# Optimization experiments

Hardware: AMD Instinct MI355X
Metric: run time of the kernel (lower is better)

The kernel has to match this reference:

```python
import jax, jax.numpy as jnp
import numpy as np

VOCAB = 4096   # vocab_size; must equal dim for weight + A@B to typecheck (as in source)
DIM = 4096
RANK = 256     # lora_rank
BATCH, SEQ = 4, 2048


def setup_inputs() -> dict:
    key = jax.random.key(0)
    k1, k2, k3, k4, k5 = jax.random.split(key, 5)
    x = jax.random.randint(k1, (BATCH, SEQ), 0, VOCAB)
    padding_mask = jax.random.randint(k2, (BATCH, SEQ), 0, 2).astype(bool)
    weight = jax.random.normal(k3, (VOCAB, DIM), dtype=jnp.float32) * 0.02
    A = jax.random.normal(k4, (VOCAB, RANK), dtype=jnp.float32) * 0.01
    B = jax.random.normal(k5, (RANK, VOCAB), dtype=jnp.float32) * 0.01
    return {"x": x, "padding_mask": padding_mask, "weight": weight, "A": A, "B": B}


def reference(x, padding_mask, weight, A, B):
    # world_size == 1, rank == 0 in the source module, so the distributed
    # index-shift / mask / all_reduce branches are no-ops.
    # lora_rank > 0 branch: embedding against the LoRA-corrected weight.
    # NOTE: faithful to source, A@B is [V, V] and requires DIM == VOCAB.
    corrected = weight + A @ B            # [V, DIM]
    y = corrected[x]                      # gather rows -> [B, S, DIM]
    # y[padding_mask] = 0
    y = jnp.where(padding_mask[..., None], jnp.zeros((), dtype=y.dtype), y)
    return y
```

## Files before the change

kernel.cpp:

```cpp
#include <hip/hip_runtime.h>
#include <stdint.h>

#define NTOK 8192
#define NCOL 4096
#define RANK 256
#define TPB  128
#define CPB  256

typedef __attribute__((ext_vector_type(8))) short bf16x8;
typedef __attribute__((ext_vector_type(4))) float f32x4;

__device__ __forceinline__ unsigned short f2bf(float f) {
    unsigned int u = __float_as_uint(f);
    u += 0x7fffu + ((u >> 16) & 1u);
    return (unsigned short)(u >> 16);
}

__global__ __launch_bounds__(256) void prep_kernel(
    const float* __restrict__ A, const float* __restrict__ B,
    unsigned short* __restrict__ Abf, unsigned short* __restrict__ Bfrag)
{
    if (blockIdx.x < 1024) {
        int i = blockIdx.x * 256 + threadIdx.x;
        float4 v = reinterpret_cast<const float4*>(A)[i];
        ushort4 o;
        o.x = f2bf(v.x); o.y = f2bf(v.y); o.z = f2bf(v.z); o.w = f2bf(v.w);
        reinterpret_cast<ushort4*>(Abf)[i] = o;
    } else {
        int gt = (blockIdx.x - 1024) * 256 + threadIdx.x;
        int ct = gt >> 9;
        int rem = gt & 511;
        int ks = rem >> 6;
        int ln = rem & 63;
        int col = ct * 16 + (ln & 15);
        int kb  = ks * 32 + ((ln >> 4) << 3);
        unsigned short pk[8];
        #pragma unroll
        for (int j = 0; j < 8; ++j)
            pk[j] = f2bf(B[(size_t)(kb + j) * NCOL + col]);
        uint4 o;
        o.x = (unsigned)pk[0] | ((unsigned)pk[1] << 16);
        o.y = (unsigned)pk[2] | ((unsigned)pk[3] << 16);
        o.z = (unsigned)pk[4] | ((unsigned)pk[5] << 16);
        o.w = (unsigned)pk[6] | ((unsigned)pk[7] << 16);
        reinterpret_cast<uint4*>(Bfrag)[gt] = o;
    }
}

__global__ __launch_bounds__(256) void emb_lora_mfma(
    const int* __restrict__ x,
    const int* __restrict__ mask,
    const float* __restrict__ W,
    const unsigned short* __restrict__ Abf,
    const unsigned short* __restrict__ Bfrag,
    float* __restrict__ out)
{
    __shared__ int s_idx[TPB];
    __shared__ int s_msk[TPB];

    const int tid  = threadIdx.x;
    const int lane = tid & 63;
    const int wave = tid >> 6;
    const int tok0 = blockIdx.x * TPB;
    const int col0 = blockIdx.y * CPB;

    if (tid < TPB) {
        s_idx[tid] = x[tok0 + tid];
        s_msk[tid] = mask[tok0 + tid];
    }
    __syncthreads();

    const int a0row = s_idx[wave * 32 + (lane & 15)];
    const int a1row = s_idx[wave * 32 + 16 + (lane & 15)];
    const unsigned short* ap0 = Abf + (size_t)a0row * RANK + ((lane >> 4) << 3);
    const unsigned short* ap1 = Abf + (size_t)a1row * RANK + ((lane >> 4) << 3);
    bf16x8 aA[8], aB[8];
    #pragma unroll
    for (int s = 0; s < 8; ++s) {
        aA[s] = *reinterpret_cast<const bf16x8*>(ap0 + s * 32);
        aB[s] = *reinterpret_cast<const bf16x8*>(ap1 + s * 32);
    }

    const int colb = col0 + (lane & 15);
    int msk0[4], msk1[4];
    unsigned woff0[4], woff1[4], ooff0[4], ooff1[4];
    #pragma unroll
    for (int r = 0; r < 4; ++r) {
        int row0 = wave * 32 + ((lane >> 4) << 2) + r;
        int row1 = row0 + 16;
        msk0[r] = s_msk[row0];
        msk1[r] = s_msk[row1];
        woff0[r] = (unsigned)s_idx[row0] * NCOL + colb;
        woff1[r] = (unsigned)s_idx[row1] * NCOL + colb;
        ooff0[r] = (unsigned)(tok0 + row0) * NCOL + colb;
        ooff1[r] = (unsigned)(tok0 + row1) * NCOL + colb;
    }

    const uint4* bcol = reinterpret_cast<const uint4*>(Bfrag)
                        + (size_t)(blockIdx.y * 16) * 512 + lane;

    float wv0[4][4], wv1[4][4];
    #pragma unroll
    for (int p = 0; p < 4; ++p) {
        #pragma unroll
        for (int r = 0; r < 4; ++r) {
            float v0 = 0.0f, v1 = 0.0f;
            if (!msk0[r]) v0 = W[woff0[r] + p * 16];
            if (!msk1[r]) v1 = W[woff1[r] + p * 16];
            wv0[p][r] = v0;
            wv1[p][r] = v1;
        }
    }

#define TILE_BODY(T, SLOT, PF)                                           \
    {                                                                    \
        const int t_ = (T);                                              \
        uint4 bb[8];                                                     \
        _Pragma("unroll")                                                \
        for (int s = 0; s < 8; ++s)                                      \
            bb[s] = bcol[t_ * 512 + s * 64];                             \
        float wc0[4], wc1[4];                                            \
        _Pragma("unroll")                                                \
        for (int r = 0; r < 4; ++r) { wc0[r] = wv0[SLOT][r]; wc1[r] = wv1[SLOT][r]; } \
        if (PF) {                                                        \
            _Pragma("unroll")                                            \
            for (int r = 0; r < 4; ++r) {                                \
                float v0 = 0.0f, v1 = 0.0f;                              \
                if (!msk0[r]) v0 = W[woff0[r] + (t_ + 4) * 16];          \
                if (!msk1[r]) v1 = W[woff1[r] + (t_ + 4) * 16];          \
                wv0[SLOT][r] = v0;                                       \
                wv1[SLOT][r] = v1;                                       \
            }                                                            \
        }                                                                \
        f32x4 acc00 = {0.f,0.f,0.f,0.f}, acc01 = {0.f,0.f,0.f,0.f};      \
        f32x4 acc10 = {0.f,0.f,0.f,0.f}, acc11 = {0.f,0.f,0.f,0.f};      \
        _Pragma("unroll")                                                \
        for (int s = 0; s < 4; ++s) {                                    \
            bf16x8 b0 = __builtin_bit_cast(bf16x8, bb[s]);               \
            bf16x8 b1 = __builtin_bit_cast(bf16x8, bb[s + 4]);           \
            acc00 = __builtin_amdgcn_mfma_f32_16x16x32_bf16(aA[s],     b0, acc00, 0, 0, 0); \
            acc01 = __builtin_amdgcn_mfma_f32_16x16x32_bf16(aA[s + 4], b1, acc01, 0, 0, 0); \
            acc10 = __builtin_amdgcn_mfma_f32_16x16x32_bf16(aB[s],     b0, acc10, 0, 0, 0); \
            acc11 = __builtin_amdgcn_mfma_f32_16x16x32_bf16(aB[s + 4], b1, acc11, 0, 0, 0); \
        }                                                                \
        _Pragma("unroll")                                                \
        for (int r = 0; r < 4; ++r) {                                    \
            float v0 = msk0[r] ? 0.0f : (acc00[r] + acc01[r] + wc0[r]);  \
            float v1 = msk1[r] ? 0.0f : (acc10[r] + acc11[r] + wc1[r]);  \
            out[ooff0[r] + t_ * 16] = v0;                                \
            out[ooff1[r] + t_ * 16] = v1;                                \
        }                                                                \
    }

    #pragma unroll 1
    for (int t0 = 0; t0 < 12; t0 += 4) {
        TILE_BODY(t0 + 0, 0, 1);
        TILE_BODY(t0 + 1, 1, 1);
        TILE_BODY(t0 + 2, 2, 1);
        TILE_BODY(t0 + 3, 3, 1);
    }
    TILE_BODY(12, 0, 0);
    TILE_BODY(13, 1, 0);
    TILE_BODY(14, 2, 0);
    TILE_BODY(15, 3, 0);
#undef TILE_BODY
}

extern "C" void kernel_launch(void* const* d_in, const int* in_sizes, int n_in,
                              void* d_out, int out_size, void* d_ws, size_t ws_size,
                              hipStream_t stream) {
    (void)in_sizes; (void)n_in; (void)out_size; (void)ws_size;

    const int*   x    = (const int*)d_in[0];
    const int*   mask = (const int*)d_in[1];
    const float* W    = (const float*)d_in[2];
    const float* A    = (const float*)d_in[3];
    const float* B    = (const float*)d_in[4];
    float*       out  = (float*)d_out;

    unsigned short* Abf   = (unsigned short*)d_ws;
    unsigned short* Bfrag = (unsigned short*)((char*)d_ws + (2u << 20));

    prep_kernel<<<dim3(1536), dim3(256), 0, stream>>>(A, B, Abf, Bfrag);

    dim3 grid(NTOK / TPB, NCOL / CPB);
    emb_lora_mfma<<<grid, dim3(256), 0, stream>>>(x, mask, W, Abf, Bfrag, out);
}
```

Baseline: 54.25 us.

## Stage B fragments through double-buffered LDS via direct global-to-LDS loads

Instead of each of the four waves loading the full B fragment tile from global memory into registers, the block cooperatively stages each 8KB B tile into shared memory with global_load_lds, double-buffered so the next tile is fetched while the current one is used. Waves then read B from LDS. This cuts redundant global/L2 traffic for B by four times. In exchange it adds a block barrier per tile and fully unrolls the tile loop, and the wave stalls at each barrier may hurt a kernel that is mostly bandwidth-bound on the W gather and output writes.

Result: faster. 52.28 us (-3.6%).

```diff
diff --git a/kernel.cpp b/kernel.cpp
--- a/kernel.cpp
+++ b/kernel.cpp
@@ -14,6 +14,12 @@
     unsigned int u = __float_as_uint(f);
     u += 0x7fffu + ((u >> 16) & 1u);
     return (unsigned short)(u >> 16);
+}
+
+__device__ __forceinline__ void gload_lds16(const uint4* g, uint4* l) {
+    __builtin_amdgcn_global_load_lds(
+        (const __attribute__((address_space(1))) void*)g,
+        (__attribute__((address_space(3))) void*)l, 16, 0, 0);
 }
 
 __global__ __launch_bounds__(256) void prep_kernel(
@@ -57,6 +63,7 @@
 {
     __shared__ int s_idx[TPB];
     __shared__ int s_msk[TPB];
+    __shared__ uint4 b_lds[2][512];
 
     const int tid  = threadIdx.x;
     const int lane = tid & 63;
@@ -96,8 +103,8 @@
         ooff1[r] = (unsigned)(tok0 + row1) * NCOL + colb;
     }
 
-    const uint4* bcol = reinterpret_cast<const uint4*>(Bfrag)
-                        + (size_t)(blockIdx.y * 16) * 512 + lane;
+    const uint4* bpanel = reinterpret_cast<const uint4*>(Bfrag)
+                          + (size_t)(blockIdx.y * 16) * 512;
 
     float wv0[4][4], wv1[4][4];
     #pragma unroll
@@ -112,13 +119,20 @@
         }
     }
 
-#define TILE_BODY(T, SLOT, PF)                                           \
+#define STAGE(T, BUF)                                                    \
+    {                                                                    \
+        const uint4* gs = bpanel + (T) * 512 + wave * 128 + lane;        \
+        gload_lds16(gs,      &b_lds[BUF][wave * 128]);                   \
+        gload_lds16(gs + 64, &b_lds[BUF][wave * 128 + 64]);              \
+    }
+
+    STAGE(0, 0);
+    __syncthreads();
+
+#define TILE_BODY(T, BUF, SLOT, PF)                                      \
     {                                                                    \
         const int t_ = (T);                                              \
-        uint4 bb[8];                                                     \
-        _Pragma("unroll")                                                \
-        for (int s = 0; s < 8; ++s)                                      \
-            bb[s] = bcol[t_ * 512 + s * 64];                             \
+        if (t_ < 15) { STAGE(t_ + 1, 1 - (BUF)); }                       \
         float wc0[4], wc1[4];                                            \
         _Pragma("unroll")                                                \
         for (int r = 0; r < 4; ++r) { wc0[r] = wv0[SLOT][r]; wc1[r] = wv1[SLOT][r]; } \
@@ -132,6 +146,10 @@
                 wv1[SLOT][r] = v1;                                       \
             }                                                            \
         }                                                                \
+        uint4 bb[8];                                                     \
+        _Pragma("unroll")                                                \
+        for (int s = 0; s < 8; ++s)                                      \
+            bb[s] = b_lds[BUF][s * 64 + lane];                           \
         f32x4 acc00 = {0.f,0.f,0.f,0.f}, acc01 = {0.f,0.f,0.f,0.f};      \
         f32x4 acc10 = {0.f,0.f,0.f,0.f}, acc11 = {0.f,0.f,0.f,0.f};      \
         _Pragma("unroll")                                                \
@@ -150,20 +168,27 @@
             out[ooff0[r] + t_ * 16] = v0;                                \
             out[ooff1[r] + t_ * 16] = v1;                                \
         }                                                                \
-    }
-
-    #pragma unroll 1
-    for (int t0 = 0; t0 < 12; t0 += 4) {
-        TILE_BODY(t0 + 0, 0, 1);
-        TILE_BODY(t0 + 1, 1, 1);
-        TILE_BODY(t0 + 2, 2, 1);
-        TILE_BODY(t0 + 3, 3, 1);
-    }
-    TILE_BODY(12, 0, 0);
-    TILE_BODY(13, 1, 0);
-    TILE_BODY(14, 2, 0);
-    TILE_BODY(15, 3, 0);
+        __syncthreads();   \
+    }
+
+    TILE_BODY(0,  0, 0, 1);
+    TILE_BODY(1,  1, 1, 1);
+    TILE_BODY(2,  0, 2, 1);
+    TILE_BODY(3,  1, 3, 1);
+    TILE_BODY(4,  0, 0, 1);
+    TILE_BODY(5,  1, 1, 1);
+    TILE_BODY(6,  0, 2, 1);
+    TILE_BODY(7,  1, 3, 1);
+    TILE_BODY(8,  0, 0, 1);
+    TILE_BODY(9,  1, 1, 1);
+    TILE_BODY(10, 0, 2, 1);
+    TILE_BODY(11, 1, 3, 1);
+    TILE_BODY(12, 0, 0, 0);
+    TILE_BODY(13, 1, 1, 0);
+    TILE_BODY(14, 0, 2, 0);
+    TILE_BODY(15, 1, 3, 0);
 #undef TILE_BODY
+#undef STAGE
 }
 
 extern "C" void kernel_launch(void* const* d_in, const int* in_sizes, int n_in,
```
